# Optimization experiments

Hardware: AMD Instinct MI355X
Metric: run time of the kernel (lower is better)

Reference implementation:

```python
import jax, jax.numpy as jnp
import numpy as np

N = 100000   # nodes
E = 1600000  # directed edges
B = 512      # graphs in batch
F = 9        # atom feature columns (OGB AtomEncoder)
V = 128      # vocab per atom feature
H = 256      # nhid
C = 10       # num_classes


def setup_inputs() -> dict:
    key = jax.random.key(0)
    ks = jax.random.split(key, 14)
    s = lambda k, shape: (jax.random.normal(k, shape, jnp.float32) * 0.05)
    return {
        "x": jax.random.randint(ks[0], (N, F), 0, V),
        "edge_index": jax.random.randint(ks[1], (2, E), 0, N),
        "batch": jnp.sort(jax.random.randint(ks[2], (N,), 0, B)),
        "atom_emb": s(ks[3], (F, V, H)),
        "W1": s(ks[4], (H, H)), "b1": s(ks[5], (H,)),
        "W2": s(ks[6], (H, H)), "b2": s(ks[7], (H,)),
        "W3": s(ks[8], (H, H)), "b3": s(ks[9], (H,)),
        "cw1": s(ks[10], (H, H // 2)), "cb1": s(ks[11], (H // 2,)),
        "cw2": s(ks[12], (H // 2, C)), "cb2": s(ks[13], (C,)),
    }


def reference(x, edge_index, batch, atom_emb, W1, b1, W2, b2, W3, b3, cw1, cb1, cw2, cb2):
    n = x.shape[0]
    # AtomEncoder: sum of per-column embeddings -> [N, H]
    h = atom_emb[jnp.arange(F)[None, :], x].sum(axis=1)

    # GCN normalization with self-loops (PyG GCNConv default)
    loop = jnp.arange(n, dtype=edge_index.dtype)
    row = jnp.concatenate([edge_index[0], loop])  # source
    col = jnp.concatenate([edge_index[1], loop])  # target
    deg = jax.ops.segment_sum(jnp.ones_like(col, jnp.float32), col, num_segments=n)
    dis = deg ** -0.5  # deg >= 1 because of self-loops
    norm = dis[row] * dis[col]  # [E+N]

    def gcn(feat, W, b):
        m = feat @ W                                   # [N, H]
        agg = jax.ops.segment_sum(norm[:, None] * m[row], col, num_segments=n)
        return agg + b

    x1 = jax.nn.relu(gcn(h, W1, b1))
    x2 = jax.nn.relu(gcn(x1, W2, b2))
    x3 = jax.nn.relu(gcn(x2, W3, b3))

    # global mean pool per graph, summed across the three layers
    counts = jax.ops.segment_sum(jnp.ones((n,), jnp.float32), batch, num_segments=B)
    pooled = jax.ops.segment_sum(x1 + x2 + x3, batch, num_segments=B) / counts[:, None]

    # classifier (dropout is identity in eval mode)
    hdn = jax.nn.relu(pooled @ cw1 + cb1)
    out = hdn @ cw2 + cb2
    return (out, 0)
```

## Files before the change

kernel.cpp:

```cpp
#include <hip/hip_runtime.h>
#include <hip/hip_bf16.h>
#include <cstdint>

#define HDIM 256
#define H2   128

using f32x4  = __attribute__((ext_vector_type(4))) float;
using bf16x8 = __attribute__((ext_vector_type(8))) short;
using u16x8  = __attribute__((ext_vector_type(8))) unsigned short;

__device__ inline unsigned short f2bf(float f) {
    unsigned x = __builtin_bit_cast(unsigned, f);
    return (unsigned short)((x + 0x7fffu + ((x >> 16) & 1u)) >> 16);
}
__device__ inline float bf2f(unsigned short u) {
    unsigned x = ((unsigned)u) << 16;
    return __builtin_bit_cast(float, x);
}

__global__ void k_init(int* __restrict__ deg, int* __restrict__ cursor,
                       float* __restrict__ pooled, int n, int bh) {
    int i = blockIdx.x * blockDim.x + threadIdx.x;
    if (i < n) { deg[i] = 1; cursor[i] = 0; }
    if (i < bh) pooled[i] = 0.f;
}

__global__ void k_deg(const int* __restrict__ col, int* __restrict__ deg, int e) {
    int i = blockIdx.x * blockDim.x + threadIdx.x;
    if (i < e) atomicAdd(&deg[col[i]], 1);
}

__global__ void k_scan1(const int* __restrict__ deg, int* __restrict__ ptr,
                        int* __restrict__ bsum, int n) {
    __shared__ int sd[256];
    int i = blockIdx.x * 256 + threadIdx.x;
    int v = (i < n) ? (deg[i] - 1) : 0;
    sd[threadIdx.x] = v;
    __syncthreads();
    for (int off = 1; off < 256; off <<= 1) {
        int t = (threadIdx.x >= off) ? sd[threadIdx.x - off] : 0;
        __syncthreads();
        sd[threadIdx.x] += t;
        __syncthreads();
    }
    if (i < n) ptr[i] = sd[threadIdx.x] - v;
    if (threadIdx.x == 255) bsum[blockIdx.x] = sd[255];
}

__global__ void k_scan2(int* __restrict__ bsum, int nb) {
    __shared__ int sd[512];
    int t = threadIdx.x;
    int v = (t < nb) ? bsum[t] : 0;
    sd[t] = v;
    __syncthreads();
    for (int off = 1; off < 512; off <<= 1) {
        int x = (t >= off) ? sd[t - off] : 0;
        __syncthreads();
        sd[t] += x;
        __syncthreads();
    }
    if (t < nb) bsum[t] = sd[t] - v;
}

__global__ void k_scan3(int* __restrict__ ptr, const int* __restrict__ bsum,
                        const int* __restrict__ deg, float* __restrict__ dis, int n) {
    int i = blockIdx.x * 256 + threadIdx.x;
    if (i < n) {
        ptr[i] += bsum[blockIdx.x];
        dis[i] = rsqrtf((float)deg[i]);
    }
}

__global__ void k_fill(const int* __restrict__ row, const int* __restrict__ col,
                       const int* __restrict__ ptr, int* __restrict__ cursor,
                       int* __restrict__ csr_src, int e) {
    int i = blockIdx.x * blockDim.x + threadIdx.x;
    if (i < e) {
        int v = col[i];
        int s = atomicAdd(&cursor[v], 1);
        csr_src[ptr[v] + s] = row[i];
    }
}

__global__ void k_counts(const int* __restrict__ batch, float* __restrict__ counts,
                         int n, int B) {
    int g = blockIdx.x * blockDim.x + threadIdx.x;
    if (g >= B) return;
    auto lb = [&](int key) {
        int lo = 0, hi = n;
        while (lo < hi) { int mid = (lo + hi) >> 1; if (batch[mid] < key) lo = mid + 1; else hi = mid; }
        return lo;
    };
    counts[g] = (float)(lb(g + 1) - lb(g));
}

__global__ __launch_bounds__(256) void k_atom(const int* __restrict__ x,
                                              const float* __restrict__ emb,
                                              short* __restrict__ h,
                                              int n, int F, int V) {
    int node = blockIdx.x * 4 + (threadIdx.x >> 6);
    int lane = threadIdx.x & 63;
    if (node >= n) return;
    int xv = x[node * F + (lane < F ? lane : 0)];
    float4 acc = {0.f, 0.f, 0.f, 0.f};
    for (int f = 0; f < F; ++f) {
        int idx = __shfl(xv, f, 64);
        const float4 v = *(const float4*)(emb + ((size_t)f * V + idx) * HDIM + lane * 4);
        acc.x += v.x; acc.y += v.y; acc.z += v.z; acc.w += v.w;
    }
    ushort4 o = { f2bf(acc.x), f2bf(acc.y), f2bf(acc.z), f2bf(acc.w) };
    *(ushort4*)(h + (size_t)node * HDIM + lane * 4) = o;
}

__global__ void k_wt3(const float* __restrict__ W1, const float* __restrict__ W2,
                      const float* __restrict__ W3, short* __restrict__ Wt1,
                      short* __restrict__ Wt2, short* __restrict__ Wt3) {
    const float* W = (blockIdx.y == 0) ? W1 : (blockIdx.y == 1) ? W2 : W3;
    short* Wt      = (blockIdx.y == 0) ? Wt1 : (blockIdx.y == 1) ? Wt2 : Wt3;
    int i = blockIdx.x * 256 + threadIdx.x;
    int nn = i >> 8, k = i & 255;
    Wt[nn * HDIM + k] = (short)f2bf(W[k * HDIM + nn]);
}

__global__ __launch_bounds__(256) void k_gemm(const short* __restrict__ A,
                                              const short* __restrict__ Wt,
                                              short* __restrict__ Co, int n) {
    int wid  = threadIdx.x >> 6;
    int lane = threadIdx.x & 63;
    int wr = wid >> 1, wc = wid & 1;
    int row0 = blockIdx.x * 128 + wr * 64;
    int col0 = wc * 128;
    int lm = lane & 15;
    int kg = lane >> 4;
    f32x4 acc[4][8] = {};
    for (int kk = 0; kk < HDIM; kk += 32) {
        bf16x8 a[4], b[8];
#pragma unroll
        for (int i = 0; i < 4; ++i) {
            int r = row0 + i * 16 + lm;
            a[i] = (r < n) ? *(const bf16x8*)(A + (size_t)r * HDIM + kk + kg * 8)
                           : (bf16x8)(short)0;
        }
#pragma unroll
        for (int j = 0; j < 8; ++j) {
            int c = col0 + j * 16 + lm;
            b[j] = *(const bf16x8*)(Wt + (size_t)c * HDIM + kk + kg * 8);
        }
#pragma unroll
        for (int i = 0; i < 4; ++i)
#pragma unroll
            for (int j = 0; j < 8; ++j)
                acc[i][j] = __builtin_amdgcn_mfma_f32_16x16x32_bf16(a[i], b[j], acc[i][j], 0, 0, 0);
    }
#pragma unroll
    for (int i = 0; i < 4; ++i)
#pragma unroll
        for (int j = 0; j < 8; ++j) {
            int c = col0 + j * 16 + lm;
#pragma unroll
            for (int r4 = 0; r4 < 4; ++r4) {
                int r = row0 + i * 16 + kg * 4 + r4;
                if (r < n) Co[(size_t)r * HDIM + c] = (short)f2bf(acc[i][j][r4]);
            }
        }
}

__global__ __launch_bounds__(256) void k_agg(const short* __restrict__ mS,
                                             const int* __restrict__ csr_src,
                                             const int* __restrict__ ptr,
                                             const int* __restrict__ deg,
                                             const float* __restrict__ dis,
                                             const float* __restrict__ bias,
                                             short* __restrict__ xout, int n) {
    int node = blockIdx.x * 4 + (threadIdx.x >> 6);
    if (node >= n) return;
    int lane = threadIdx.x & 63;
    int half = lane >> 5;
    int cl = lane & 31;
    const unsigned short* m = (const unsigned short*)mS;
    float dv = dis[node];
    float acc[8] = {};
    if (half == 0) {
        u16x8 r = *(const u16x8*)(m + (size_t)node * HDIM + cl * 8);
        float sw = dv * dv;
#pragma unroll
        for (int j = 0; j < 8; ++j) acc[j] = sw * bf2f(r[j]);
    }
    int start = ptr[node];
    int cnt = deg[node] - 1;
    for (int base = 0; base < cnt; base += 64) {
        int mm = cnt - base; if (mm > 64) mm = 64;
        int uu = 0; float du = 0.f;
        if (lane < mm) {
            uu = __builtin_nontemporal_load(&csr_src[start + base + lane]);
            du = dis[uu];
        }
        int nst = (mm + 7) >> 3;
        for (int s = 0; s < nst; ++s) {
            u16x8 r[4]; float w[4];
#pragma unroll
            for (int q = 0; q < 4; ++q) {
                int i = 8 * s + 2 * q + half;
                int u   = __shfl(uu, i & 63, 64);
                float ww = dv * __shfl(du, i & 63, 64);
                bool v = i < mm;
                w[q] = v ? ww : 0.f;
                r[q] = *(const u16x8*)(m + (size_t)(v ? u : 0) * HDIM + cl * 8);
            }
#pragma unroll
            for (int q = 0; q < 4; ++q)
#pragma unroll
                for (int j = 0; j < 8; ++j) acc[j] += w[q] * bf2f(r[q][j]);
        }
    }
#pragma unroll
    for (int j = 0; j < 8; ++j) acc[j] += __shfl_xor(acc[j], 32, 64);
    if (half == 0) {
        const float4 b0 = *(const float4*)(bias + cl * 8);
        const float4 b1 = *(const float4*)(bias + cl * 8 + 4);
        float bb[8] = {b0.x, b0.y, b0.z, b0.w, b1.x, b1.y, b1.z, b1.w};
        u16x8 o;
#pragma unroll
        for (int j = 0; j < 8; ++j)
            o[j] = f2bf(fmaxf(acc[j] + bb[j], 0.f));
        *(u16x8*)((unsigned short*)xout + (size_t)node * HDIM + cl * 8) = o;
    }
}

__global__ __launch_bounds__(256) void k_pool(const short* __restrict__ x1,
                                              const short* __restrict__ x2,
                                              const short* __restrict__ x3,
                                              const int* __restrict__ batch,
                                              float* __restrict__ pooled, int n) {
    int g = blockIdx.x, seg = blockIdx.y, t = threadIdx.x;
    auto lb = [&](int key) {
        int lo = 0, hi = n;
        while (lo < hi) { int mid = (lo + hi) >> 1; if (batch[mid] < key) lo = mid + 1; else hi = mid; }
        return lo;
    };
    int lo = lb(g), hi = lb(g + 1);
    int len = hi - lo;
    int per = (len + (int)gridDim.y - 1) / (int)gridDim.y;
    int s0 = lo + seg * per;
    int s1 = s0 + per; if (s1 > hi) s1 = hi;
    float acc = 0.f;
    for (int r = s0; r < s1; ++r) {
        size_t base = (size_t)r * HDIM + t;
        acc += bf2f((unsigned short)x1[base]) + bf2f((unsigned short)x2[base])
             + bf2f((unsigned short)x3[base]);
    }
    if (s0 < s1) atomicAdd(&pooled[g * HDIM + t], acc);
}

__global__ __launch_bounds__(H2) void k_cls(const float* __restrict__ pooled,
                                            const float* __restrict__ counts,
                                            const float* __restrict__ cw1,
                                            const float* __restrict__ cb1,
                                            const float* __restrict__ cw2,
                                            const float* __restrict__ cb2,
                                            float* __restrict__ out, int B, int C) {
    __shared__ float sp[HDIM];
    __shared__ float sh[H2];
    int g = blockIdx.x, t = threadIdx.x;
    float inv = 1.0f / counts[g];
    sp[t] = pooled[g * HDIM + t] * inv;
    sp[t + H2] = pooled[g * HDIM + t + H2] * inv;
    __syncthreads();
    float acc = cb1[t];
    for (int h = 0; h < HDIM; ++h) acc += sp[h] * cw1[h * H2 + t];
    sh[t] = fmaxf(acc, 0.f);
    __syncthreads();
    if (t < C) {
        float o = cb2[t];
        for (int j = 0; j < H2; ++j) o += sh[j] * cw2[j * C + t];
        out[g * C + t] = o;
    }
    if (g == 0 && t == 0) out[B * C] = 0.f;
}

extern "C" void kernel_launch(void* const* d_in, const int* in_sizes, int n_in,
                              void* d_out, int out_size, void* d_ws, size_t ws_size,
                              hipStream_t stream) {
    const int* x      = (const int*)d_in[0];
    const int* erow   = (const int*)d_in[1];
    const int* batch  = (const int*)d_in[2];
    const float* emb  = (const float*)d_in[3];
    const float* W1   = (const float*)d_in[4];
    const float* b1   = (const float*)d_in[5];
    const float* W2   = (const float*)d_in[6];
    const float* b2   = (const float*)d_in[7];
    const float* W3   = (const float*)d_in[8];
    const float* b3   = (const float*)d_in[9];
    const float* cw1  = (const float*)d_in[10];
    const float* cb1  = (const float*)d_in[11];
    const float* cw2  = (const float*)d_in[12];
    const float* cb2  = (const float*)d_in[13];
    float* out = (float*)d_out;

    const int N = in_sizes[2];
    const int E = in_sizes[1] / 2;
    const int F = in_sizes[0] / N;
    const int V = in_sizes[3] / (F * HDIM);
    const int C = in_sizes[13];
    const int B = (out_size - 1) / C;
    const int* ecol = erow + E;

    char* w = (char*)d_ws;
    auto carve = [&](size_t bytes) {
        void* p = (void*)w;
        w += (bytes + 255) & ~(size_t)255;
        return p;
    };
    short* P0     = (short*)carve((size_t)N * HDIM * 2);
    short* P1     = (short*)carve((size_t)N * HDIM * 2);
    short* P2     = (short*)carve((size_t)N * HDIM * 2);
    short* mS     = (short*)carve((size_t)N * HDIM * 2);
    short* Wt1    = (short*)carve((size_t)HDIM * HDIM * 2);
    short* Wt2    = (short*)carve((size_t)HDIM * HDIM * 2);
    short* Wt3    = (short*)carve((size_t)HDIM * HDIM * 2);
    float* dis    = (float*)carve((size_t)N * 4);
    float* pooled = (float*)carve((size_t)B * HDIM * 4);
    float* counts = (float*)carve((size_t)B * 4);
    int* deg      = (int*)carve((size_t)N * 4);
    int* ptr      = (int*)carve((size_t)N * 4);
    int* cursor   = (int*)carve((size_t)N * 4);
    int* bsum     = (int*)carve(1024 * 4);
    int* csr      = (int*)carve((size_t)E * 4);

    int nblk = (N + 255) / 256;
    int initspan = (B * HDIM > N) ? B * HDIM : N;

    k_init<<<(initspan + 255) / 256, 256, 0, stream>>>(deg, cursor, pooled, N, B * HDIM);
    k_deg<<<(E + 255) / 256, 256, 0, stream>>>(ecol, deg, E);
    k_scan1<<<nblk, 256, 0, stream>>>(deg, ptr, bsum, N);
    k_scan2<<<1, 512, 0, stream>>>(bsum, nblk);
    k_scan3<<<nblk, 256, 0, stream>>>(ptr, bsum, deg, dis, N);
    k_fill<<<(E + 255) / 256, 256, 0, stream>>>(erow, ecol, ptr, cursor, csr, E);
    k_counts<<<(B + 255) / 256, 256, 0, stream>>>(batch, counts, N, B);
    dim3 wgrid(HDIM, 3);
    k_wt3<<<wgrid, 256, 0, stream>>>(W1, W2, W3, Wt1, Wt2, Wt3);
    k_atom<<<(N + 3) / 4, 256, 0, stream>>>(x, emb, P0, N, F, V);

    int ggrid = (N + 127) / 128;
    int agrid = (N + 3) / 4;

    k_gemm<<<ggrid, 256, 0, stream>>>(P0, Wt1, mS, N);
    k_agg<<<agrid, 256, 0, stream>>>(mS, csr, ptr, deg, dis, b1, P1, N);
    k_gemm<<<ggrid, 256, 0, stream>>>(P1, Wt2, mS, N);
    k_agg<<<agrid, 256, 0, stream>>>(mS, csr, ptr, deg, dis, b2, P2, N);
    k_gemm<<<ggrid, 256, 0, stream>>>(P2, Wt3, mS, N);
    k_agg<<<agrid, 256, 0, stream>>>(mS, csr, ptr, deg, dis, b3, P0, N);

    dim3 pgrid(B, 4);
    k_pool<<<pgrid, 256, 0, stream>>>(P1, P2, P0, batch, pooled, N);
    k_cls<<<B, H2, 0, stream>>>(pooled, counts, cw1, cb1, cw2, cb2, out, B, C);
}
```

Before: 838.4 us.

## Stage GEMM A tile in swizzled LDS and use 8 waves per block

```diff
diff --git a/kernel.cpp b/kernel.cpp
--- a/kernel.cpp
+++ b/kernel.cpp
@@ -122,44 +122,59 @@
     Wt[nn * HDIM + k] = (short)f2bf(W[k * HDIM + nn]);
 }
 
-__global__ __launch_bounds__(256) void k_gemm(const short* __restrict__ A,
-                                              const short* __restrict__ Wt,
-                                              short* __restrict__ Co, int n) {
-    int wid  = threadIdx.x >> 6;
-    int lane = threadIdx.x & 63;
-    int wr = wid >> 1, wc = wid & 1;
-    int row0 = blockIdx.x * 128 + wr * 64;
-    int col0 = wc * 128;
+__global__ __launch_bounds__(512, 4) void k_gemm(const short* __restrict__ A,
+                                                 const short* __restrict__ Wt,
+                                                 short* __restrict__ Co, int n) {
+    __shared__ unsigned char As[128 * 512];
+    int row0 = blockIdx.x * 128;
+    int t = threadIdx.x;
+    const unsigned short* A16 = (const unsigned short*)A;
+#pragma unroll
+    for (int j = 0; j < 8; ++j) {
+        int c = j * 512 + t;
+        int r = c >> 5;
+        int wb = (c & 31) * 16;
+        int gr = row0 + r; if (gr >= n) gr = n - 1;
+        u16x8 v = *(const u16x8*)(A16 + (size_t)gr * HDIM + (wb >> 1));
+        *(u16x8*)(As + r * 512 + (wb ^ ((r & 7) << 4))) = v;
+    }
+    __syncthreads();
+
+    int wid  = t >> 6;
+    int lane = t & 63;
+    int wr = wid >> 2, wc = wid & 3;
     int lm = lane & 15;
     int kg = lane >> 4;
-    f32x4 acc[4][8] = {};
-    for (int kk = 0; kk < HDIM; kk += 32) {
-        bf16x8 a[4], b[8];
+    int colw = wc * 64;
+    f32x4 acc[4][4] = {};
+#pragma unroll 2
+    for (int kk = 0; kk < 8; ++kk) {
+        bf16x8 a[4], b[4];
 #pragma unroll
         for (int i = 0; i < 4; ++i) {
-            int r = row0 + i * 16 + lm;
-            a[i] = (r < n) ? *(const bf16x8*)(A + (size_t)r * HDIM + kk + kg * 8)
-                           : (bf16x8)(short)0;
-        }
-#pragma unroll
-        for (int j = 0; j < 8; ++j) {
-            int c = col0 + j * 16 + lm;
-            b[j] = *(const bf16x8*)(Wt + (size_t)c * HDIM + kk + kg * 8);
+            int R = wr * 64 + i * 16 + lm;
+            int boff = (kk * 64 + kg * 16) ^ ((R & 7) << 4);
+            a[i] = *(const bf16x8*)(As + R * 512 + boff);
+        }
+#pragma unroll
+        for (int j = 0; j < 4; ++j) {
+            int cidx = colw + j * 16 + lm;
+            b[j] = *(const bf16x8*)(Wt + (size_t)cidx * HDIM + kk * 32 + kg * 8);
         }
 #pragma unroll
         for (int i = 0; i < 4; ++i)
 #pragma unroll
-            for (int j = 0; j < 8; ++j)
+            for (int j = 0; j < 4; ++j)
                 acc[i][j] = __builtin_amdgcn_mfma_f32_16x16x32_bf16(a[i], b[j], acc[i][j], 0, 0, 0);
     }
 #pragma unroll
     for (int i = 0; i < 4; ++i)
 #pragma unroll
-        for (int j = 0; j < 8; ++j) {
-            int c = col0 + j * 16 + lm;
+        for (int j = 0; j < 4; ++j) {
+            int c = colw + j * 16 + lm;
 #pragma unroll
             for (int r4 = 0; r4 < 4; ++r4) {
-                int r = row0 + i * 16 + kg * 4 + r4;
+                int r = row0 + wr * 64 + i * 16 + kg * 4 + r4;
                 if (r < n) Co[(size_t)r * HDIM + c] = (short)f2bf(acc[i][j][r4]);
             }
         }
@@ -344,11 +359,11 @@
     int ggrid = (N + 127) / 128;
     int agrid = (N + 3) / 4;
 
-    k_gemm<<<ggrid, 256, 0, stream>>>(P0, Wt1, mS, N);
+    k_gemm<<<ggrid, 512, 0, stream>>>(P0, Wt1, mS, N);
     k_agg<<<agrid, 256, 0, stream>>>(mS, csr, ptr, deg, dis, b1, P1, N);
-    k_gemm<<<ggrid, 256, 0, stream>>>(P1, Wt2, mS, N);
+    k_gemm<<<ggrid, 512, 0, stream>>>(P1, Wt2, mS, N);
     k_agg<<<agrid, 256, 0, stream>>>(mS, csr, ptr, deg, dis, b2, P2, N);
-    k_gemm<<<ggrid, 256, 0, stream>>>(P2, Wt3, mS, N);
+    k_gemm<<<ggrid, 512, 0, stream>>>(P2, Wt3, mS, N);
     k_agg<<<agrid, 256, 0, stream>>>(mS, csr, ptr, deg, dis, b3, P0, N);
 
     dim3 pgrid(B, 4);
```

After: 780.6 us. 1.07x faster.
